# Kernel optimization log

Hardware: AMD Instinct MI355X
Metric: run time of the kernel (lower is better)

## Reference

```python
import jax, jax.numpy as jnp
import numpy as np

NUM_WORDS = 100000
D_IN = 256

def setup_inputs() -> dict:
    key = jax.random.key(0)
    k1, k2 = jax.random.split(key)
    x = jax.random.normal(k1, (NUM_WORDS, D_IN), dtype=jnp.float32)
    # neighbor indices in [-1, NUM_WORDS); -1 means 'no neighbor' (masked out)
    indices = jax.random.randint(k2, (NUM_WORDS, 4), -1, NUM_WORDS, dtype=jnp.int64)
    return {"x": x, "indices": indices}

def reference(x, indices):
    # x: [N, D], indices: [N, 4] int (-1 -> masked neighbor)
    mask = (indices != -1)                               # [N, 4]
    safe_idx = jnp.maximum(indices, 0)                   # clamp -1 -> 0 like np.maximum in source
    gathered = x[safe_idx]                               # [N, 4, D]
    gathered = gathered * mask[..., None].astype(x.dtype)
    n, d = x.shape
    return jnp.concatenate([x, gathered.reshape(n, 4 * d)], axis=1)  # [N, 5*D]
```

## Files before the change

kernel.cpp:

```cpp
#include <hip/hip_runtime.h>


typedef float f32x4 __attribute__((ext_vector_type(4)));

#define D 256
#define D4 (D / 4)
#define OUTW (5 * D)
#define OUTW4 (OUTW / 4)
#define ROWS_PER_BLOCK 4

__global__ __launch_bounds__(256) void collect_kernel(
    const f32x4* __restrict__ x4,
    const int*   __restrict__ indices,
    f32x4*       __restrict__ out4,
    int n)
{
    const int wave = threadIdx.x >> 6;
    const int lane = threadIdx.x & 63;
    const int row  = blockIdx.x * ROWS_PER_BLOCK + wave;
    if (row >= n) return;

    const f32x4* xrow = x4 + (long)row * D4;
    f32x4* orow = out4 + (long)row * OUTW4;

    const int i0 = indices[row * 4 + 0];
    const int i1 = indices[row * 4 + 1];
    const int i2 = indices[row * 4 + 2];
    const int i3 = indices[row * 4 + 3];

    const f32x4 zero = (f32x4){0.f, 0.f, 0.f, 0.f};

    f32x4 v_self = xrow[lane];
    f32x4 v0 = (i0 >= 0) ? x4[(long)i0 * D4 + lane] : zero;
    f32x4 v1 = (i1 >= 0) ? x4[(long)i1 * D4 + lane] : zero;
    f32x4 v2 = (i2 >= 0) ? x4[(long)i2 * D4 + lane] : zero;
    f32x4 v3 = (i3 >= 0) ? x4[(long)i3 * D4 + lane] : zero;

    __builtin_nontemporal_store(v_self, &orow[lane]);
    __builtin_nontemporal_store(v0, &orow[D4 * 1 + lane]);
    __builtin_nontemporal_store(v1, &orow[D4 * 2 + lane]);
    __builtin_nontemporal_store(v2, &orow[D4 * 3 + lane]);
    __builtin_nontemporal_store(v3, &orow[D4 * 4 + lane]);
}

extern "C" void kernel_launch(void* const* d_in, const int* in_sizes, int n_in,
                              void* d_out, int out_size, void* d_ws, size_t ws_size,
                              hipStream_t stream)
{
    const f32x4* x4 = (const f32x4*)d_in[0];
    const int* indices = (const int*)d_in[1];
    f32x4* out4 = (f32x4*)d_out;

    const int n = in_sizes[0] / D;

    dim3 block(256);
    dim3 grid((n + ROWS_PER_BLOCK - 1) / ROWS_PER_BLOCK);
    collect_kernel<<<grid, block, 0, stream>>>(x4, indices, out4, n);
}
```

Before: 149.8 us.

## Replace gather with inverted-index scatter so each source row is read once

Builds per-target buckets of referencing (row, slot) pairs with atomics, then each wave reads its own x row once and writes it to its self slot and to every output slot that references it, while zeroing masked slots. An overflow list and fixup kernel handle targets with more than the bucket capacity, and the old gather kernel is kept as a fallback when workspace is too small. This aims to cut the random gather reads of x, which is already L2/MALL-resident, in exchange for four kernel launches, atomic contention, bucket reads, and scattered writes.

```diff
diff --git a/kernel.cpp b/kernel.cpp
--- a/kernel.cpp
+++ b/kernel.cpp
@@ -5,37 +5,107 @@
 
 #define D 256
 #define D4 (D / 4)
-#define OUTW (5 * D)
-#define OUTW4 (OUTW / 4)
-#define ROWS_PER_BLOCK 4
+#define OUTW4 (5 * D / 4)
+#define CAP 16
+#define OVF_CAP 65536
 
-__global__ __launch_bounds__(256) void collect_kernel(
+__global__ __launch_bounds__(256) void zero_counts_kernel(int* counts, int* ovf_cnt, int n)
+{
+    int i = blockIdx.x * blockDim.x + threadIdx.x;
+    if (i == 0) *ovf_cnt = 0;
+    if (i < n) counts[i] = 0;
+}
+
+__global__ __launch_bounds__(256) void build_buckets_kernel(
+    const int* __restrict__ indices, int* counts, int* buckets,
+    int* ovf, int* ovf_cnt, int n4)
+{
+    int e = blockIdx.x * blockDim.x + threadIdx.x;
+    if (e >= n4) return;
+    int t = indices[e];
+    if (t < 0) return;
+    int pos = atomicAdd(&counts[t], 1);
+    if (pos < CAP) {
+        buckets[t * CAP + pos] = e;
+    } else {
+        int o = atomicAdd(ovf_cnt, 1);
+        if (o < OVF_CAP) ovf[o] = e;
+    }
+}
+
+__global__ __launch_bounds__(256) void scatter_kernel(
     const f32x4* __restrict__ x4,
     const int*   __restrict__ indices,
+    const int*   __restrict__ counts,
+    const int*   __restrict__ buckets,
     f32x4*       __restrict__ out4,
     int n)
 {
     const int wave = threadIdx.x >> 6;
     const int lane = threadIdx.x & 63;
-    const int row  = blockIdx.x * ROWS_PER_BLOCK + wave;
+    const int r = blockIdx.x * 4 + wave;
+    if (r >= n) return;
+
+    const f32x4 v = __builtin_nontemporal_load(&x4[(long)r * D4 + lane]);
+
+    __builtin_nontemporal_store(v, &out4[(long)r * OUTW4 + lane]);
+
+    const f32x4 zero = (f32x4){0.f, 0.f, 0.f, 0.f};
+    #pragma unroll
+    for (int s = 0; s < 4; ++s) {
+        if (indices[r * 4 + s] < 0)
+            __builtin_nontemporal_store(zero, &out4[(long)r * OUTW4 + (1 + s) * D4 + lane]);
+    }
+
+    int cnt = counts[r];
+    if (cnt > CAP) cnt = CAP;
+    for (int j = 0; j < cnt; ++j) {
+        int e = buckets[r * CAP + j];
+        int dest = e >> 2, slot = e & 3;
+        __builtin_nontemporal_store(v, &out4[(long)dest * OUTW4 + (1 + slot) * D4 + lane]);
+    }
+}
+
+__global__ __launch_bounds__(256) void overflow_fixup_kernel(
+    const f32x4* __restrict__ x4, const int* __restrict__ indices,
+    const int* __restrict__ ovf, const int* __restrict__ ovf_cnt,
+    f32x4* __restrict__ out4)
+{
+    const int wave = threadIdx.x >> 6;
+    const int lane = threadIdx.x & 63;
+    const int gw = blockIdx.x * 4 + wave;
+    const int nwaves = gridDim.x * 4;
+    int cnt = *ovf_cnt;
+    if (cnt > OVF_CAP) cnt = OVF_CAP;
+    for (int i = gw; i < cnt; i += nwaves) {
+        int e = ovf[i];
+        int row = e >> 2, slot = e & 3;
+        int t = indices[e];
+        f32x4 v = x4[(long)t * D4 + lane];
+        __builtin_nontemporal_store(v, &out4[(long)row * OUTW4 + (1 + slot) * D4 + lane]);
+    }
+}
+
+__global__ __launch_bounds__(256) void collect_fwd_kernel(
+    const f32x4* __restrict__ x4, const int* __restrict__ indices,
+    f32x4* __restrict__ out4, int n)
+{
+    const int wave = threadIdx.x >> 6;
+    const int lane = threadIdx.x & 63;
+    const int row  = blockIdx.x * 4 + wave;
     if (row >= n) return;
-
     const f32x4* xrow = x4 + (long)row * D4;
     f32x4* orow = out4 + (long)row * OUTW4;
-
     const int i0 = indices[row * 4 + 0];
     const int i1 = indices[row * 4 + 1];
     const int i2 = indices[row * 4 + 2];
     const int i3 = indices[row * 4 + 3];
-
     const f32x4 zero = (f32x4){0.f, 0.f, 0.f, 0.f};
-
     f32x4 v_self = xrow[lane];
     f32x4 v0 = (i0 >= 0) ? x4[(long)i0 * D4 + lane] : zero;
     f32x4 v1 = (i1 >= 0) ? x4[(long)i1 * D4 + lane] : zero;
     f32x4 v2 = (i2 >= 0) ? x4[(long)i2 * D4 + lane] : zero;
     f32x4 v3 = (i3 >= 0) ? x4[(long)i3 * D4 + lane] : zero;
-
     __builtin_nontemporal_store(v_self, &orow[lane]);
     __builtin_nontemporal_store(v0, &orow[D4 * 1 + lane]);
     __builtin_nontemporal_store(v1, &orow[D4 * 2 + lane]);
@@ -51,9 +121,33 @@
     const int* indices = (const int*)d_in[1];
     f32x4* out4 = (f32x4*)d_out;
 
-    const int n = in_sizes[0] / D;
+    const int n  = in_sizes[0] / D;
+    const int n4 = in_sizes[1];
+
+    size_t off_counts  = 0;
+    size_t off_ovfcnt  = (size_t)((n * 4 + 63) / 64) * 64;
+    size_t off_ovf     = off_ovfcnt + 64;
+    size_t off_buckets = off_ovf + (size_t)OVF_CAP * 4;
+    size_t need = off_buckets + (size_t)n * CAP * 4;
 
     dim3 block(256);
-    dim3 grid((n + ROWS_PER_BLOCK - 1) / ROWS_PER_BLOCK);
-    collect_kernel<<<grid, block, 0, stream>>>(x4, indices, out4, n);
+
+    if (ws_size < need) {
+        collect_fwd_kernel<<<dim3((n + 3) / 4), block, 0, stream>>>(x4, indices, out4, n);
+        return;
+    }
+
+    char* ws = (char*)d_ws;
+    int* counts  = (int*)(ws + off_counts);
+    int* ovf_cnt = (int*)(ws + off_ovfcnt);
+    int* ovf     = (int*)(ws + off_ovf);
+    int* buckets = (int*)(ws + off_buckets);
+
+    zero_counts_kernel<<<dim3((n + 255) / 256), block, 0, stream>>>(counts, ovf_cnt, n);
+    build_buckets_kernel<<<dim3((n4 + 255) / 256), block, 0, stream>>>(
+        indices, counts, buckets, ovf, ovf_cnt, n4);
+    scatter_kernel<<<dim3((n + 3) / 4), block, 0, stream>>>(
+        x4, indices, counts, buckets, out4, n);
+    overflow_fixup_kernel<<<dim3(8), block, 0, stream>>>(
+        x4, indices, ovf, ovf_cnt, out4);
 }
```

Result: faster. 145.7 us (median of 2 runs) (-2.7%).

## Bucket gather edges by source segment and scatter per segment for locality

Applied to the files above, without the earlier changes.

Replaces the single fused gather kernel with a multi-kernel pipeline. Edges (destination slot, source row) are bucketed into 16 source-row segments in a workspace buffer. A separate kernel copies the self rows and zero-fills masked slots, and a final kernel processes edges segment by segment, so gathers from x land in a smaller working set that should stay cache-resident. The cost is extra kernel launches, atomics, an edge-buffer round trip and many empty blocks in the scatter grid. Edges beyond a fixed per-segment capacity would be silently dropped.

```diff
diff --git a/kernel.cpp b/kernel.cpp
--- a/kernel.cpp
+++ b/kernel.cpp
@@ -5,37 +5,109 @@
 
 #define D 256
 #define D4 (D / 4)
-#define OUTW (5 * D)
-#define OUTW4 (OUTW / 4)
-#define ROWS_PER_BLOCK 4
+#define OUTW4 (5 * D / 4)
+#define S 16
+#define BPS 8192
+#define CAP (BPS * 4)
 
-__global__ __launch_bounds__(256) void collect_kernel(
-    const f32x4* __restrict__ x4,
-    const int*   __restrict__ indices,
-    f32x4*       __restrict__ out4,
-    int n)
+__global__ __launch_bounds__(64) void zero_counts_kernel(int* seg_cnt)
+{
+    if (threadIdx.x < S) seg_cnt[threadIdx.x] = 0;
+}
+
+__global__ __launch_bounds__(256) void build_edges_kernel(
+    const int* __restrict__ indices, int n4, int segrows,
+    int* seg_cnt, uint2* __restrict__ ebuf)
+{
+    __shared__ int lcnt[S];
+    __shared__ int lbase[S];
+    if (threadIdx.x < S) lcnt[threadIdx.x] = 0;
+    __syncthreads();
+
+    const int e = blockIdx.x * 256 + threadIdx.x;
+    int t = -1, seg = 0, pos = 0;
+    if (e < n4) t = indices[e];
+    if (t >= 0) {
+        seg = t / segrows;
+        pos = atomicAdd(&lcnt[seg], 1);
+    }
+    __syncthreads();
+    if (threadIdx.x < S) {
+        int c = lcnt[threadIdx.x];
+        lbase[threadIdx.x] = c ? atomicAdd(&seg_cnt[threadIdx.x], c) : 0;
+    }
+    __syncthreads();
+    if (t >= 0) {
+        int p = lbase[seg] + pos;
+        if (p < CAP)
+            ebuf[(long)seg * CAP + p] = make_uint2((unsigned)e, (unsigned)t);
+    }
+}
+
+__global__ __launch_bounds__(256) void self_copy_kernel(
+    const f32x4* __restrict__ x4, const int* __restrict__ indices,
+    f32x4* __restrict__ out4, int n)
 {
     const int wave = threadIdx.x >> 6;
     const int lane = threadIdx.x & 63;
-    const int row  = blockIdx.x * ROWS_PER_BLOCK + wave;
+    const int row  = blockIdx.x * 4 + wave;
     if (row >= n) return;
 
+    f32x4 v = __builtin_nontemporal_load(&x4[(long)row * D4 + lane]);
+    __builtin_nontemporal_store(v, &out4[(long)row * OUTW4 + lane]);
+
+    const f32x4 zero = (f32x4){0.f, 0.f, 0.f, 0.f};
+    #pragma unroll
+    for (int s = 0; s < 4; ++s) {
+        if (indices[row * 4 + s] < 0)
+            __builtin_nontemporal_store(zero,
+                &out4[(long)row * OUTW4 + (1 + s) * D4 + lane]);
+    }
+}
+
+__global__ __launch_bounds__(256) void edge_scatter_kernel(
+    const f32x4* __restrict__ x4, const int* __restrict__ seg_cnt,
+    const uint2* __restrict__ ebuf, f32x4* __restrict__ out4)
+{
+    const int wv   = threadIdx.x >> 6;
+    const int lane = threadIdx.x & 63;
+    const int seg    = blockIdx.x >> 13;
+    const int within = blockIdx.x & (BPS - 1);
+    const int eidx = within * 4 + wv;
+
+    int cnt = seg_cnt[seg];
+    if (cnt > CAP) cnt = CAP;
+    if (eidx >= cnt) return;
+
+    const uint2 ed = ebuf[(long)seg * CAP + eidx];
+    const int e = (int)ed.x, src = (int)ed.y;
+    const int dest = e >> 2, slot = e & 3;
+
+    f32x4 v = x4[(long)src * D4 + lane];
+    __builtin_nontemporal_store(v,
+        &out4[(long)dest * OUTW4 + (1 + slot) * D4 + lane]);
+}
+
+__global__ __launch_bounds__(256) void collect_fwd_kernel(
+    const f32x4* __restrict__ x4, const int* __restrict__ indices,
+    f32x4* __restrict__ out4, int n)
+{
+    const int wave = threadIdx.x >> 6;
+    const int lane = threadIdx.x & 63;
+    const int row  = blockIdx.x * 4 + wave;
+    if (row >= n) return;
     const f32x4* xrow = x4 + (long)row * D4;
     f32x4* orow = out4 + (long)row * OUTW4;
-
     const int i0 = indices[row * 4 + 0];
     const int i1 = indices[row * 4 + 1];
     const int i2 = indices[row * 4 + 2];
     const int i3 = indices[row * 4 + 3];
-
     const f32x4 zero = (f32x4){0.f, 0.f, 0.f, 0.f};
-
     f32x4 v_self = xrow[lane];
     f32x4 v0 = (i0 >= 0) ? x4[(long)i0 * D4 + lane] : zero;
     f32x4 v1 = (i1 >= 0) ? x4[(long)i1 * D4 + lane] : zero;
     f32x4 v2 = (i2 >= 0) ? x4[(long)i2 * D4 + lane] : zero;
     f32x4 v3 = (i3 >= 0) ? x4[(long)i3 * D4 + lane] : zero;
-
     __builtin_nontemporal_store(v_self, &orow[lane]);
     __builtin_nontemporal_store(v0, &orow[D4 * 1 + lane]);
     __builtin_nontemporal_store(v1, &orow[D4 * 2 + lane]);
@@ -51,9 +123,28 @@
     const int* indices = (const int*)d_in[1];
     f32x4* out4 = (f32x4*)d_out;
 
-    const int n = in_sizes[0] / D;
+    const int n  = in_sizes[0] / D;
+    const int n4 = in_sizes[1];
+    const int segrows = (n + S - 1) / S;
+
+    size_t off_cnt  = 0;
+    size_t off_ebuf = 64;
+    size_t need = off_ebuf + (size_t)S * CAP * sizeof(uint2);
 
     dim3 block(256);
-    dim3 grid((n + ROWS_PER_BLOCK - 1) / ROWS_PER_BLOCK);
-    collect_kernel<<<grid, block, 0, stream>>>(x4, indices, out4, n);
+
+    if (ws_size < need) {
+        collect_fwd_kernel<<<dim3((n + 3) / 4), block, 0, stream>>>(x4, indices, out4, n);
+        return;
+    }
+
+    char* ws = (char*)d_ws;
+    int*   seg_cnt = (int*)(ws + off_cnt);
+    uint2* ebuf    = (uint2*)(ws + off_ebuf);
+
+    zero_counts_kernel<<<dim3(1), dim3(64), 0, stream>>>(seg_cnt);
+    build_edges_kernel<<<dim3((n4 + 255) / 256), block, 0, stream>>>(
+        indices, n4, segrows, seg_cnt, ebuf);
+    self_copy_kernel<<<dim3((n + 3) / 4), block, 0, stream>>>(x4, indices, out4, n);
+    edge_scatter_kernel<<<dim3(S * BPS), block, 0, stream>>>(x4, seg_cnt, ebuf, out4);
 }
```

Result: slower. 196.3 us (+31.0%).
